# Kernel optimization log

Hardware: AMD Instinct MI355X
Metric: run time of the kernel (lower is better)

The kernel has to match this reference:

```python
import jax, jax.numpy as jnp
import numpy as np

B, S, E, FFN, Q = 8, 2048, 512, 2048, 8


def setup_inputs() -> dict:
    key = jax.random.key(0)
    k0, k1, k2, k3 = jax.random.split(key, 4)
    x = jax.random.normal(k0, (B, S, E), dtype=jnp.float32)
    ry = jax.random.normal(k1, (Q,), dtype=jnp.float32)  # trainable RY angles
    w1 = jax.random.normal(k2, (FFN, Q), dtype=jnp.float32) / np.sqrt(Q).astype(np.float32)
    b1 = jnp.zeros((FFN,), dtype=jnp.float32)
    w2 = jax.random.normal(k3, (E, FFN), dtype=jnp.float32) / np.sqrt(FFN).astype(np.float32)
    b2 = jnp.zeros((E,), dtype=jnp.float32)
    return {"x": x, "ry": ry, "w1": w1, "b1": b1, "w2": w2, "b2": b2}


def reference(x, ry, w1, b1, w2, b2):
    # Quantum layer: each qubit i starts in |0>, gets RX(x[..., i]) then RY(ry[i]),
    # then PauliZ expectation. Product state => closed form <Z_i> = cos(x_i) * cos(ry_i).
    nq = ry.shape[0]
    z = jnp.cos(x[..., :nq]) * jnp.cos(ry)  # [B, S, Q]
    # dropout is identity in eval mode
    h = jnp.einsum("bsq,fq->bsf", z, w1) + b1  # fc1
    return jnp.einsum("bsf,ef->bse", jax.nn.relu(h), w2) + b2  # fc2
```

## Files before the change

kernel.cpp:

```cpp
#include <hip/hip_runtime.h>
#include <cstdint>
#include <cstddef>


typedef __attribute__((ext_vector_type(8))) short s16x8;
typedef __attribute__((ext_vector_type(4))) float f32x4;

__device__ __forceinline__ unsigned short f2bf(float f) {
  unsigned int u = __float_as_uint(f);
  unsigned int r = u + 0x7fffu + ((u >> 16) & 1u);
  return (unsigned short)(r >> 16);
}

__device__ __forceinline__ void async_copy16(const void* g, void* l) {
  __builtin_amdgcn_global_load_lds(
      (const __attribute__((address_space(1))) void*)(uintptr_t)g,
      (__attribute__((address_space(3))) void*)(unsigned int)(uintptr_t)l,
      16, 0, 0);
}

__global__ __launch_bounds__(256) void k_w2(const float* __restrict__ w2,
                                            unsigned short* __restrict__ w2b) {
  size_t i = ((size_t)blockIdx.x * 256 + threadIdx.x) * 4;
  float4 v = *(const float4*)(w2 + i);
  uint2 p;
  p.x = f2bf(v.x) | ((unsigned)f2bf(v.y) << 16);
  p.y = f2bf(v.z) | ((unsigned)f2bf(v.w) << 16);
  *(uint2*)(w2b + i) = p;
}

__global__ __launch_bounds__(512) void k_fused(
    const float* __restrict__ x, const float* __restrict__ ry,
    const float* __restrict__ w1, const float* __restrict__ b1,
    const unsigned short* __restrict__ w2b, const float* __restrict__ b2,
    float* __restrict__ C) {
  __shared__ unsigned short As[128 * 32];
  __shared__ unsigned short Bs[256 * 32];
  __shared__ float w1s[2][8][32];
  __shared__ float b1s[2048];

  const int t = threadIdx.x;
  const int lane = t & 63;
  const int w = t >> 6;
  const int mt = (int)(blockIdx.x >> 1);
  const int nt = (int)(blockIdx.x & 1);
  const int r0 = mt * 128;
  const int c0 = nt * 256;

  const int arow = t >> 2;
  const int k8 = (t & 3) * 8;

  float z[8];
  {
    const float* xr = x + (size_t)(r0 + arow) * 512;
    float4 x0 = *(const float4*)xr;
    float4 x1 = *(const float4*)(xr + 4);
    float4 ra = *(const float4*)ry;
    float4 rb = *(const float4*)(ry + 4);
    z[0] = __cosf(x0.x) * __cosf(ra.x);
    z[1] = __cosf(x0.y) * __cosf(ra.y);
    z[2] = __cosf(x0.z) * __cosf(ra.z);
    z[3] = __cosf(x0.w) * __cosf(ra.w);
    z[4] = __cosf(x1.x) * __cosf(rb.x);
    z[5] = __cosf(x1.y) * __cosf(rb.y);
    z[6] = __cosf(x1.z) * __cosf(rb.z);
    z[7] = __cosf(x1.w) * __cosf(rb.w);
  }
  {
    float4 v = *(const float4*)(b1 + t * 4);
    *(float4*)&b1s[t * 4] = v;
  }
  if (t < 64) {
    float4 v = *(const float4*)(w1 + t * 4);
    const int fl = t >> 1, q0 = (t & 1) * 4;
    w1s[0][q0 + 0][fl] = v.x;
    w1s[0][q0 + 1][fl] = v.y;
    w1s[0][q0 + 2][fl] = v.z;
    w1s[0][q0 + 3][fl] = v.w;
  }
  __syncthreads();

  const unsigned short* gB1 =
      w2b + (size_t)(c0 + (t >> 2)) * 2048 + (t & 3) * 8;
  const unsigned short* gB2 = gB1 + (size_t)128 * 2048;
  char* lB1 = (char*)Bs + t * 16;
  char* lB2 = lB1 + 512 * 16;

  const int wm = (w >> 2) * 64;
  const int wn = (w & 3) * 64;
  const int fr = lane & 15;
  const int quad = lane >> 4;

  f32x4 acc[4][4];
#pragma unroll
  for (int i = 0; i < 4; ++i)
#pragma unroll
    for (int j = 0; j < 4; ++j) acc[i][j] = (f32x4){0.f, 0.f, 0.f, 0.f};

  const unsigned short* pAf = As + (wm + fr) * 32 + quad * 8;
  const unsigned short* pBf = Bs + (wn + fr) * 32 + quad * 8;
  unsigned short* pAw = As + arow * 32 + k8;

  for (int kt = 0; kt < 64; ++kt) {
    const int cur = kt & 1;

    async_copy16(gB1, lB1);
    async_copy16(gB2, lB2);
    gB1 += 32;
    gB2 += 32;
    float4 wpre;
    const bool do_w1 = (t < 64) && (kt < 63);
    if (do_w1) wpre = *(const float4*)(w1 + (kt + 1) * 256 + t * 4);

    float h[8];
    {
      float4 b0 = *(const float4*)&b1s[kt * 32 + k8];
      float4 b4 = *(const float4*)&b1s[kt * 32 + k8 + 4];
      h[0] = b0.x; h[1] = b0.y; h[2] = b0.z; h[3] = b0.w;
      h[4] = b4.x; h[5] = b4.y; h[6] = b4.z; h[7] = b4.w;
    }
#pragma unroll
    for (int q = 0; q < 8; ++q) {
      float4 wa = *(const float4*)&w1s[cur][q][k8];
      float4 wb = *(const float4*)&w1s[cur][q][k8 + 4];
      h[0] += z[q] * wa.x; h[1] += z[q] * wa.y;
      h[2] += z[q] * wa.z; h[3] += z[q] * wa.w;
      h[4] += z[q] * wb.x; h[5] += z[q] * wb.y;
      h[6] += z[q] * wb.z; h[7] += z[q] * wb.w;
    }
    unsigned short o[8];
#pragma unroll
    for (int j = 0; j < 8; ++j) o[j] = f2bf(fmaxf(h[j], 0.0f));
    uint4 pk;
    pk.x = o[0] | ((unsigned)o[1] << 16);
    pk.y = o[2] | ((unsigned)o[3] << 16);
    pk.z = o[4] | ((unsigned)o[5] << 16);
    pk.w = o[6] | ((unsigned)o[7] << 16);
    *(uint4*)pAw = pk;
    if (do_w1) {
      const int fl = t >> 1, q0 = (t & 1) * 4;
      const int nxt = cur ^ 1;
      w1s[nxt][q0 + 0][fl] = wpre.x;
      w1s[nxt][q0 + 1][fl] = wpre.y;
      w1s[nxt][q0 + 2][fl] = wpre.z;
      w1s[nxt][q0 + 3][fl] = wpre.w;
    }
    __syncthreads();

    s16x8 af[4], bfv[4];
#pragma unroll
    for (int i = 0; i < 4; ++i) af[i] = *(const s16x8*)(pAf + i * 16 * 32);
#pragma unroll
    for (int j = 0; j < 4; ++j) bfv[j] = *(const s16x8*)(pBf + j * 16 * 32);
#pragma unroll
    for (int i = 0; i < 4; ++i)
#pragma unroll
      for (int j = 0; j < 4; ++j)
        acc[i][j] = __builtin_amdgcn_mfma_f32_16x16x32_bf16(af[i], bfv[j],
                                                            acc[i][j], 0, 0, 0);
    __syncthreads();
  }

  float bias[4];
#pragma unroll
  for (int j = 0; j < 4; ++j) bias[j] = b2[c0 + wn + j * 16 + fr];
#pragma unroll
  for (int i = 0; i < 4; ++i) {
    const int rbase = r0 + wm + i * 16 + quad * 4;
#pragma unroll
    for (int rr = 0; rr < 4; ++rr) {
      float* crow = C + (size_t)(rbase + rr) * 512;
#pragma unroll
      for (int j = 0; j < 4; ++j)
        crow[c0 + wn + j * 16 + fr] = acc[i][j][rr] + bias[j];
    }
  }
}

__global__ __launch_bounds__(256) void k_naive(
    const float* __restrict__ x, const float* __restrict__ ry,
    const float* __restrict__ w1, const float* __restrict__ b1,
    const float* __restrict__ w2, const float* __restrict__ b2,
    float* __restrict__ out) {
  __shared__ float zsh[8];
  __shared__ float acts[2048];
  const int r = blockIdx.x;
  const int t = threadIdx.x;
  if (t < 8) zsh[t] = __cosf(x[(size_t)r * 512 + t]) * __cosf(ry[t]);
  __syncthreads();
  float z[8];
#pragma unroll
  for (int q = 0; q < 8; ++q) z[q] = zsh[q];
#pragma unroll
  for (int i = 0; i < 8; ++i) {
    const int f = t * 8 + i;
    const float* wr = w1 + (size_t)f * 8;
    float4 a = *(const float4*)wr;
    float4 b = *(const float4*)(wr + 4);
    float h = b1[f] + z[0] * a.x + z[1] * a.y + z[2] * a.z + z[3] * a.w +
              z[4] * b.x + z[5] * b.y + z[6] * b.z + z[7] * b.w;
    acts[f] = fmaxf(h, 0.0f);
  }
  __syncthreads();
  for (int ee = 0; ee < 2; ++ee) {
    const int e = t + ee * 256;
    const float* wr = w2 + (size_t)e * 2048;
    float acc = b2[e];
    for (int f = 0; f < 2048; f += 4) {
      float4 wv = *(const float4*)(wr + f);
      float4 av = *(const float4*)(acts + f);
      acc += av.x * wv.x + av.y * wv.y + av.z * wv.z + av.w * wv.w;
    }
    out[(size_t)r * 512 + e] = acc;
  }
}

extern "C" void kernel_launch(void* const* d_in, const int* in_sizes, int n_in,
                              void* d_out, int out_size, void* d_ws,
                              size_t ws_size, hipStream_t stream) {
  const float* x  = (const float*)d_in[0];
  const float* ry = (const float*)d_in[1];
  const float* w1 = (const float*)d_in[2];
  const float* b1 = (const float*)d_in[3];
  const float* w2 = (const float*)d_in[4];
  const float* b2 = (const float*)d_in[5];
  float* out = (float*)d_out;

  const size_t w2b_bytes = (size_t)512 * 2048 * 2;
  if (ws_size < w2b_bytes) {
    k_naive<<<dim3(16384), dim3(256), 0, stream>>>(x, ry, w1, b1, w2, b2, out);
    return;
  }
  unsigned short* w2b = (unsigned short*)d_ws;
  k_w2<<<dim3(1024), dim3(256), 0, stream>>>(w2, w2b);
  k_fused<<<dim3(256), dim3(512), 0, stream>>>(x, ry, w1, b1, w2b, b2, out);
}
```

Before: 168.4 us.

## Double-buffer A/B tiles and halve block M-tile to 64 rows with 256 threads

Restructures the fused kernel to use 64-row tiles with 256 threads (4 waves each covering 64 columns) and launches 512 blocks at two blocks per CU. A and B LDS tiles are now double-buffered, so the async W2 load and the fc1 activation compute for the next K slice overlap the MFMAs on the current slice. This cuts the loop from two barriers per iteration to one. The w1 slice layout is also changed to float4 entries. W2 is re-read by twice as many blocks, which adds L2 traffic.

```diff
diff --git a/kernel.cpp b/kernel.cpp
--- a/kernel.cpp
+++ b/kernel.cpp
@@ -29,14 +29,14 @@
   *(uint2*)(w2b + i) = p;
 }
 
-__global__ __launch_bounds__(512) void k_fused(
+__global__ __launch_bounds__(256, 2) void k_fused(
     const float* __restrict__ x, const float* __restrict__ ry,
     const float* __restrict__ w1, const float* __restrict__ b1,
     const unsigned short* __restrict__ w2b, const float* __restrict__ b2,
     float* __restrict__ C) {
-  __shared__ unsigned short As[128 * 32];
-  __shared__ unsigned short Bs[256 * 32];
-  __shared__ float w1s[2][8][32];
+  __shared__ unsigned short As[2][64 * 32];
+  __shared__ unsigned short Bs[2][256 * 32];
+  __shared__ float4 w1s[2][8][8];
   __shared__ float b1s[2048];
 
   const int t = threadIdx.x;
@@ -44,11 +44,12 @@
   const int w = t >> 6;
   const int mt = (int)(blockIdx.x >> 1);
   const int nt = (int)(blockIdx.x & 1);
-  const int r0 = mt * 128;
+  const int r0 = mt * 64;
   const int c0 = nt * 256;
 
   const int arow = t >> 2;
   const int k8 = (t & 3) * 8;
+  const int k4 = (t & 3) * 2;
 
   float z[8];
   {
@@ -67,27 +68,63 @@
     z[7] = __cosf(x1.w) * __cosf(rb.w);
   }
   {
-    float4 v = *(const float4*)(b1 + t * 4);
-    *(float4*)&b1s[t * 4] = v;
-  }
-  if (t < 64) {
-    float4 v = *(const float4*)(w1 + t * 4);
-    const int fl = t >> 1, q0 = (t & 1) * 4;
-    w1s[0][q0 + 0][fl] = v.x;
-    w1s[0][q0 + 1][fl] = v.y;
-    w1s[0][q0 + 2][fl] = v.z;
-    w1s[0][q0 + 3][fl] = v.w;
-  }
-  __syncthreads();
-
-  const unsigned short* gB1 =
+    const float4* bsrc = (const float4*)b1;
+    ((float4*)b1s)[t * 2] = bsrc[t * 2];
+    ((float4*)b1s)[t * 2 + 1] = bsrc[t * 2 + 1];
+  }
+  auto w1_stage = [&](int slice, int buf) {
+    float4 v = *(const float4*)(w1 + slice * 256 + t * 4);
+    float* dst = (float*)&w1s[buf][(t & 1) * 4][0];
+    const int fl = t >> 1;
+    dst[fl] = v.x;
+    dst[32 + fl] = v.y;
+    dst[64 + fl] = v.z;
+    dst[96 + fl] = v.w;
+  };
+  if (t < 64) w1_stage(0, 0);
+
+  const unsigned short* gB0 =
       w2b + (size_t)(c0 + (t >> 2)) * 2048 + (t & 3) * 8;
-  const unsigned short* gB2 = gB1 + (size_t)128 * 2048;
-  char* lB1 = (char*)Bs + t * 16;
-  char* lB2 = lB1 + 512 * 16;
-
-  const int wm = (w >> 2) * 64;
-  const int wn = (w & 3) * 64;
+  char* lB0 = (char*)&Bs[0][0] + t * 16;
+  auto stage_Bs = [&](int slice, int buf) {
+    const unsigned short* g = gB0 + slice * 32;
+    char* l = lB0 + buf * 16384;
+#pragma unroll
+    for (int p = 0; p < 4; ++p)
+      async_copy16(g + p * 131072, l + p * 4096);
+  };
+
+  char* aswr = (char*)&As[0][0] + arow * 64 + k8 * 2;
+  auto act = [&](int slice, int buf) {
+    const float* bp = b1s + slice * 32 + k8;
+    float4 hb0 = *(const float4*)bp;
+    float4 hb1 = *(const float4*)(bp + 4);
+    float h0 = hb0.x, h1 = hb0.y, h2 = hb0.z, h3 = hb0.w;
+    float h4 = hb1.x, h5 = hb1.y, h6 = hb1.z, h7 = hb1.w;
+#pragma unroll
+    for (int q = 0; q < 8; ++q) {
+      float4 wa = w1s[buf][q][k4];
+      float4 wb = w1s[buf][q][k4 + 1];
+      h0 += z[q] * wa.x; h1 += z[q] * wa.y;
+      h2 += z[q] * wa.z; h3 += z[q] * wa.w;
+      h4 += z[q] * wb.x; h5 += z[q] * wb.y;
+      h6 += z[q] * wb.z; h7 += z[q] * wb.w;
+    }
+    uint4 pk;
+    pk.x = f2bf(fmaxf(h0, 0.f)) | ((unsigned)f2bf(fmaxf(h1, 0.f)) << 16);
+    pk.y = f2bf(fmaxf(h2, 0.f)) | ((unsigned)f2bf(fmaxf(h3, 0.f)) << 16);
+    pk.z = f2bf(fmaxf(h4, 0.f)) | ((unsigned)f2bf(fmaxf(h5, 0.f)) << 16);
+    pk.w = f2bf(fmaxf(h6, 0.f)) | ((unsigned)f2bf(fmaxf(h7, 0.f)) << 16);
+    *(uint4*)(aswr + buf * 4096) = pk;
+  };
+
+  stage_Bs(0, 0);
+  __syncthreads();
+  act(0, 0);
+  if (t < 64) w1_stage(1, 1);
+  __syncthreads();
+
+  const int wn = w * 64;
   const int fr = lane & 15;
   const int quad = lane >> 4;
 
@@ -97,61 +134,27 @@
 #pragma unroll
     for (int j = 0; j < 4; ++j) acc[i][j] = (f32x4){0.f, 0.f, 0.f, 0.f};
 
-  const unsigned short* pAf = As + (wm + fr) * 32 + quad * 8;
-  const unsigned short* pBf = Bs + (wn + fr) * 32 + quad * 8;
-  unsigned short* pAw = As + arow * 32 + k8;
+  const char* asbase = (const char*)&As[0][0] + fr * 64 + quad * 16;
+  const char* bsbase = (const char*)&Bs[0][0] + (wn + fr) * 64 + quad * 16;
 
   for (int kt = 0; kt < 64; ++kt) {
     const int cur = kt & 1;
-
-    async_copy16(gB1, lB1);
-    async_copy16(gB2, lB2);
-    gB1 += 32;
-    gB2 += 32;
-    float4 wpre;
-    const bool do_w1 = (t < 64) && (kt < 63);
-    if (do_w1) wpre = *(const float4*)(w1 + (kt + 1) * 256 + t * 4);
-
-    float h[8];
-    {
-      float4 b0 = *(const float4*)&b1s[kt * 32 + k8];
-      float4 b4 = *(const float4*)&b1s[kt * 32 + k8 + 4];
-      h[0] = b0.x; h[1] = b0.y; h[2] = b0.z; h[3] = b0.w;
-      h[4] = b4.x; h[5] = b4.y; h[6] = b4.z; h[7] = b4.w;
-    }
-#pragma unroll
-    for (int q = 0; q < 8; ++q) {
-      float4 wa = *(const float4*)&w1s[cur][q][k8];
-      float4 wb = *(const float4*)&w1s[cur][q][k8 + 4];
-      h[0] += z[q] * wa.x; h[1] += z[q] * wa.y;
-      h[2] += z[q] * wa.z; h[3] += z[q] * wa.w;
-      h[4] += z[q] * wb.x; h[5] += z[q] * wb.y;
-      h[6] += z[q] * wb.z; h[7] += z[q] * wb.w;
-    }
-    unsigned short o[8];
-#pragma unroll
-    for (int j = 0; j < 8; ++j) o[j] = f2bf(fmaxf(h[j], 0.0f));
-    uint4 pk;
-    pk.x = o[0] | ((unsigned)o[1] << 16);
-    pk.y = o[2] | ((unsigned)o[3] << 16);
-    pk.z = o[4] | ((unsigned)o[5] << 16);
-    pk.w = o[6] | ((unsigned)o[7] << 16);
-    *(uint4*)pAw = pk;
-    if (do_w1) {
-      const int fl = t >> 1, q0 = (t & 1) * 4;
-      const int nxt = cur ^ 1;
-      w1s[nxt][q0 + 0][fl] = wpre.x;
-      w1s[nxt][q0 + 1][fl] = wpre.y;
-      w1s[nxt][q0 + 2][fl] = wpre.z;
-      w1s[nxt][q0 + 3][fl] = wpre.w;
-    }
-    __syncthreads();
+    const int nxt = cur ^ 1;
+    if (kt < 63) stage_Bs(kt + 1, nxt);
 
     s16x8 af[4], bfv[4];
 #pragma unroll
-    for (int i = 0; i < 4; ++i) af[i] = *(const s16x8*)(pAf + i * 16 * 32);
-#pragma unroll
-    for (int j = 0; j < 4; ++j) bfv[j] = *(const s16x8*)(pBf + j * 16 * 32);
+    for (int i = 0; i < 4; ++i)
+      af[i] = *(const s16x8*)(asbase + cur * 4096 + i * 1024);
+#pragma unroll
+    for (int j = 0; j < 4; ++j)
+      bfv[j] = *(const s16x8*)(bsbase + cur * 16384 + j * 1024);
+
+    if (kt < 63) {
+      act(kt + 1, nxt);
+      if (t < 64 && kt < 62) w1_stage(kt + 2, cur);
+    }
+
 #pragma unroll
     for (int i = 0; i < 4; ++i)
 #pragma unroll
@@ -166,7 +169,7 @@
   for (int j = 0; j < 4; ++j) bias[j] = b2[c0 + wn + j * 16 + fr];
 #pragma unroll
   for (int i = 0; i < 4; ++i) {
-    const int rbase = r0 + wm + i * 16 + quad * 4;
+    const int rbase = r0 + i * 16 + quad * 4;
 #pragma unroll
     for (int rr = 0; rr < 4; ++rr) {
       float* crow = C + (size_t)(rbase + rr) * 512;
@@ -233,5 +236,5 @@
   }
   unsigned short* w2b = (unsigned short*)d_ws;
   k_w2<<<dim3(1024), dim3(256), 0, stream>>>(w2, w2b);
-  k_fused<<<dim3(256), dim3(512), 0, stream>>>(x, ry, w1, b1, w2b, b2, out);
-}
+  k_fused<<<dim3(512), dim3(256), 0, stream>>>(x, ry, w1, b1, w2b, b2, out);
+}
```

After: 181.0 us. +7.5%, slower.

## Double-buffer A/B tiles with async prefetch and overlap fc1 compute with MFMA

Applied to the files above, without the earlier changes.

Both the A (activation) and B (w2 bf16) LDS tiles are now double-buffered. B tiles are prefetched two k-steps ahead with async global-to-LDS copies, and fc1 activations for the next step are computed while the current MFMAs run. All of w1 and b1 is loaded into LDS once at the start, and each thread computes 4 rows by 2 features using a hardware packed bf16 convert. Occupancy is hinted at 2 blocks per CU, which may not hold given the larger LDS footprint of roughly 120KB. Hand-placed waitcnt and barrier instructions replace __syncthreads, which risks subtle ordering errors.

```diff
diff --git a/kernel.cpp b/kernel.cpp
--- a/kernel.cpp
+++ b/kernel.cpp
@@ -29,14 +29,14 @@
   *(uint2*)(w2b + i) = p;
 }
 
-__global__ __launch_bounds__(512) void k_fused(
+__global__ __launch_bounds__(512, 2) void k_fused(
     const float* __restrict__ x, const float* __restrict__ ry,
     const float* __restrict__ w1, const float* __restrict__ b1,
     const unsigned short* __restrict__ w2b, const float* __restrict__ b2,
     float* __restrict__ C) {
-  __shared__ unsigned short As[128 * 32];
-  __shared__ unsigned short Bs[256 * 32];
-  __shared__ float w1s[2][8][32];
+  __shared__ unsigned short As[2][128 * 32];
+  __shared__ unsigned short Bs[2][256 * 32];
+  __shared__ float w1s[2048 * 8];
   __shared__ float b1s[2048];
 
   const int t = threadIdx.x;
@@ -46,45 +46,78 @@
   const int nt = (int)(blockIdx.x & 1);
   const int r0 = mt * 128;
   const int c0 = nt * 256;
-
-  const int arow = t >> 2;
-  const int k8 = (t & 3) * 8;
-
-  float z[8];
+  const int fp = t & 15;
+  const int rq = t >> 4;
+
+  const unsigned short* gB =
+      w2b + (size_t)(c0 + (t >> 2)) * 2048 + (t & 3) * 8;
+  char* lB = (char*)Bs + t * 16;
+  async_copy16(gB, lB);
+  async_copy16(gB + (size_t)128 * 2048, lB + 8192);
+#pragma unroll
+  for (int i = 0; i < 8; ++i)
+    async_copy16(w1 + ((size_t)t + i * 512) * 4,
+                 (char*)w1s + ((size_t)t + i * 512) * 16);
+  async_copy16(b1 + (size_t)t * 4, (char*)b1s + (size_t)t * 16);
+  async_copy16(gB + 32, lB + 16384);
+  async_copy16(gB + 32 + (size_t)128 * 2048, lB + 16384 + 8192);
+
+  float zr[4][8];
   {
-    const float* xr = x + (size_t)(r0 + arow) * 512;
-    float4 x0 = *(const float4*)xr;
-    float4 x1 = *(const float4*)(xr + 4);
     float4 ra = *(const float4*)ry;
     float4 rb = *(const float4*)(ry + 4);
-    z[0] = __cosf(x0.x) * __cosf(ra.x);
-    z[1] = __cosf(x0.y) * __cosf(ra.y);
-    z[2] = __cosf(x0.z) * __cosf(ra.z);
-    z[3] = __cosf(x0.w) * __cosf(ra.w);
-    z[4] = __cosf(x1.x) * __cosf(rb.x);
-    z[5] = __cosf(x1.y) * __cosf(rb.y);
-    z[6] = __cosf(x1.z) * __cosf(rb.z);
-    z[7] = __cosf(x1.w) * __cosf(rb.w);
-  }
-  {
-    float4 v = *(const float4*)(b1 + t * 4);
-    *(float4*)&b1s[t * 4] = v;
-  }
-  if (t < 64) {
-    float4 v = *(const float4*)(w1 + t * 4);
-    const int fl = t >> 1, q0 = (t & 1) * 4;
-    w1s[0][q0 + 0][fl] = v.x;
-    w1s[0][q0 + 1][fl] = v.y;
-    w1s[0][q0 + 2][fl] = v.z;
-    w1s[0][q0 + 3][fl] = v.w;
-  }
-  __syncthreads();
-
-  const unsigned short* gB1 =
-      w2b + (size_t)(c0 + (t >> 2)) * 2048 + (t & 3) * 8;
-  const unsigned short* gB2 = gB1 + (size_t)128 * 2048;
-  char* lB1 = (char*)Bs + t * 16;
-  char* lB2 = lB1 + 512 * 16;
+    float cy[8] = {__cosf(ra.x), __cosf(ra.y), __cosf(ra.z), __cosf(ra.w),
+                   __cosf(rb.x), __cosf(rb.y), __cosf(rb.z), __cosf(rb.w)};
+#pragma unroll
+    for (int r = 0; r < 4; ++r) {
+      const float* xr = x + (size_t)(r0 + rq * 4 + r) * 512;
+      float4 x0 = *(const float4*)xr;
+      float4 x1 = *(const float4*)(xr + 4);
+      zr[r][0] = __cosf(x0.x) * cy[0];
+      zr[r][1] = __cosf(x0.y) * cy[1];
+      zr[r][2] = __cosf(x0.z) * cy[2];
+      zr[r][3] = __cosf(x0.w) * cy[3];
+      zr[r][4] = __cosf(x1.x) * cy[4];
+      zr[r][5] = __cosf(x1.y) * cy[5];
+      zr[r][6] = __cosf(x1.z) * cy[6];
+      zr[r][7] = __cosf(x1.w) * cy[7];
+    }
+  }
+
+  asm volatile("s_waitcnt vmcnt(0) lgkmcnt(0)" ::: "memory");
+  __builtin_amdgcn_sched_barrier(0);
+  __builtin_amdgcn_s_barrier();
+
+  char* aswr = (char*)As + (size_t)rq * 4 * 64 + fp * 4;
+  auto act = [&](int s, int b) {
+    const float* wrow = w1s + ((size_t)s * 32 + fp * 2) * 8;
+    f32x4 v0 = *(const f32x4*)(wrow);
+    f32x4 v1 = *(const f32x4*)(wrow + 4);
+    f32x4 v2 = *(const f32x4*)(wrow + 8);
+    f32x4 v3 = *(const f32x4*)(wrow + 12);
+    float b0 = b1s[s * 32 + fp * 2];
+    float b1v = b1s[s * 32 + fp * 2 + 1];
+    char* dst = aswr + b * 8192;
+#pragma unroll
+    for (int r = 0; r < 4; ++r) {
+      float h0 = b0, h1 = b1v;
+      h0 += zr[r][0] * v0[0]; h1 += zr[r][0] * v2[0];
+      h0 += zr[r][1] * v0[1]; h1 += zr[r][1] * v2[1];
+      h0 += zr[r][2] * v0[2]; h1 += zr[r][2] * v2[2];
+      h0 += zr[r][3] * v0[3]; h1 += zr[r][3] * v2[3];
+      h0 += zr[r][4] * v1[0]; h1 += zr[r][4] * v3[0];
+      h0 += zr[r][5] * v1[1]; h1 += zr[r][5] * v3[1];
+      h0 += zr[r][6] * v1[2]; h1 += zr[r][6] * v3[2];
+      h0 += zr[r][7] * v1[3]; h1 += zr[r][7] * v3[3];
+      h0 = fmaxf(h0, 0.0f);
+      h1 = fmaxf(h1, 0.0f);
+      unsigned int u;
+      asm("v_cvt_pk_bf16_f32 %0, %1, %2" : "=v"(u) : "v"(h0), "v"(h1));
+      *(unsigned int*)(dst + r * 64) = u;
+    }
+  };
+
+  act(0, 0);
 
   const int wm = (w >> 2) * 64;
   const int wn = (w & 3) * 64;
@@ -97,68 +130,43 @@
 #pragma unroll
     for (int j = 0; j < 4; ++j) acc[i][j] = (f32x4){0.f, 0.f, 0.f, 0.f};
 
-  const unsigned short* pAf = As + (wm + fr) * 32 + quad * 8;
-  const unsigned short* pBf = Bs + (wn + fr) * 32 + quad * 8;
-  unsigned short* pAw = As + arow * 32 + k8;
+  const char* pAb = (const char*)As + (size_t)(wm + fr) * 64 + quad * 16;
+  const char* pBb = (const char*)Bs + (size_t)(wn + fr) * 64 + quad * 16;
 
   for (int kt = 0; kt < 64; ++kt) {
     const int cur = kt & 1;
 
-    async_copy16(gB1, lB1);
-    async_copy16(gB2, lB2);
-    gB1 += 32;
-    gB2 += 32;
-    float4 wpre;
-    const bool do_w1 = (t < 64) && (kt < 63);
-    if (do_w1) wpre = *(const float4*)(w1 + (kt + 1) * 256 + t * 4);
-
-    float h[8];
-    {
-      float4 b0 = *(const float4*)&b1s[kt * 32 + k8];
-      float4 b4 = *(const float4*)&b1s[kt * 32 + k8 + 4];
-      h[0] = b0.x; h[1] = b0.y; h[2] = b0.z; h[3] = b0.w;
-      h[4] = b4.x; h[5] = b4.y; h[6] = b4.z; h[7] = b4.w;
-    }
-#pragma unroll
-    for (int q = 0; q < 8; ++q) {
-      float4 wa = *(const float4*)&w1s[cur][q][k8];
-      float4 wb = *(const float4*)&w1s[cur][q][k8 + 4];
-      h[0] += z[q] * wa.x; h[1] += z[q] * wa.y;
-      h[2] += z[q] * wa.z; h[3] += z[q] * wa.w;
-      h[4] += z[q] * wb.x; h[5] += z[q] * wb.y;
-      h[6] += z[q] * wb.z; h[7] += z[q] * wb.w;
-    }
-    unsigned short o[8];
-#pragma unroll
-    for (int j = 0; j < 8; ++j) o[j] = f2bf(fmaxf(h[j], 0.0f));
-    uint4 pk;
-    pk.x = o[0] | ((unsigned)o[1] << 16);
-    pk.y = o[2] | ((unsigned)o[3] << 16);
-    pk.z = o[4] | ((unsigned)o[5] << 16);
-    pk.w = o[6] | ((unsigned)o[7] << 16);
-    *(uint4*)pAw = pk;
-    if (do_w1) {
-      const int fl = t >> 1, q0 = (t & 1) * 4;
-      const int nxt = cur ^ 1;
-      w1s[nxt][q0 + 0][fl] = wpre.x;
-      w1s[nxt][q0 + 1][fl] = wpre.y;
-      w1s[nxt][q0 + 2][fl] = wpre.z;
-      w1s[nxt][q0 + 3][fl] = wpre.w;
-    }
-    __syncthreads();
+    asm volatile("s_waitcnt vmcnt(2) lgkmcnt(0)" ::: "memory");
+    __builtin_amdgcn_sched_barrier(0);
+    __builtin_amdgcn_s_barrier();
 
     s16x8 af[4], bfv[4];
-#pragma unroll
-    for (int i = 0; i < 4; ++i) af[i] = *(const s16x8*)(pAf + i * 16 * 32);
-#pragma unroll
-    for (int j = 0; j < 4; ++j) bfv[j] = *(const s16x8*)(pBf + j * 16 * 32);
+    const char* pA = pAb + cur * 8192;
+    const char* pB = pBb + cur * 16384;
+#pragma unroll
+    for (int i = 0; i < 4; ++i) af[i] = *(const s16x8*)(pA + i * 1024);
+#pragma unroll
+    for (int j = 0; j < 4; ++j) bfv[j] = *(const s16x8*)(pB + j * 1024);
+
+    if (kt < 63) act(kt + 1, cur ^ 1);
+
 #pragma unroll
     for (int i = 0; i < 4; ++i)
 #pragma unroll
       for (int j = 0; j < 4; ++j)
         acc[i][j] = __builtin_amdgcn_mfma_f32_16x16x32_bf16(af[i], bfv[j],
                                                             acc[i][j], 0, 0, 0);
-    __syncthreads();
+
+    asm volatile("s_waitcnt lgkmcnt(0)" ::: "memory");
+    __builtin_amdgcn_sched_barrier(0);
+    __builtin_amdgcn_s_barrier();
+
+    if (kt < 62) {
+      const unsigned short* g = gB + (kt + 2) * 32;
+      char* l = lB + cur * 16384;
+      async_copy16(g, l);
+      async_copy16(g + (size_t)128 * 2048, l + 8192);
+    }
   }
 
   float bias[4];
```

Measured after the change: 151.3 us. 10.2% less time.
